# Performance work log

Hardware: AMD Instinct MI355X
Metric: run time of the kernel (lower is better)

## Reference

```python
import jax, jax.numpy as jnp
import numpy as np

B, S, I, H, O = 64, 2048, 128, 256, 128


def setup_inputs() -> dict:
    key = jax.random.key(0)
    ks = jax.random.split(key, 7)
    s = 1.0 / np.sqrt(H)
    return {
        "x": jax.random.normal(ks[0], (B, S, I), dtype=jnp.float32),
        "W_ih": jax.random.uniform(ks[1], (H, I), jnp.float32, -s, s),
        "W_hh": jax.random.uniform(ks[2], (H, H), jnp.float32, -s, s),
        "b_ih": jax.random.uniform(ks[3], (H,), jnp.float32, -s, s),
        "b_hh": jax.random.uniform(ks[4], (H,), jnp.float32, -s, s),
        "W_fc": jax.random.uniform(ks[5], (O, H), jnp.float32, -s, s),
        "b_fc": jax.random.uniform(ks[6], (O,), jnp.float32, -s, s),
    }


def reference(x, W_ih, W_hh, b_ih, b_hh, W_fc, b_fc):
    # h_t = tanh(x_t @ W_ih^T + h_{t-1} @ W_hh^T + b_ih + b_hh)
    b = b_ih + b_hh
    # Precompute input projection for all timesteps in one GEMM: [B,S,H]
    xproj = jnp.einsum('bsi,hi->bsh', x, W_ih) + b

    def step(h, xp_t):  # h: [B,H], xp_t: [B,H]
        h_next = jnp.tanh(xp_t + h @ W_hh.T)
        return h_next, h_next

    h0 = jnp.zeros((B, H), dtype=x.dtype)
    _, hs = jax.lax.scan(step, h0, jnp.swapaxes(xproj, 0, 1))  # hs: [S,B,H]
    hidden_states = jnp.swapaxes(hs, 0, 1)  # [B,S,H]
    outputs = jnp.einsum('bsh,oh->bso', hidden_states, W_fc) + b_fc  # [B,S,O]
    return outputs, hidden_states
```

## Files before the change

kernel.cpp:

```cpp
#include <hip/hip_runtime.h>

#define BB 64
#define SS 2048
#define II 128
#define HH 256
#define OO 128

typedef _Float16 h2_t __attribute__((ext_vector_type(2)));

__device__ __forceinline__ h2_t u2h(unsigned u) {
    union { unsigned u; h2_t h; } c; c.u = u; return c.h;
}

#if __has_builtin(__builtin_amdgcn_fdot2)
__device__ __forceinline__ float fdot2(unsigned h, unsigned w, float acc) {
    return __builtin_amdgcn_fdot2(u2h(h), u2h(w), acc, false);
}
#else
__device__ __forceinline__ float fdot2(unsigned h, unsigned w, float acc) {
    h2_t hh = u2h(h), ww = u2h(w);
    acc = fmaf((float)hh.x, (float)ww.x, acc);
    acc = fmaf((float)hh.y, (float)ww.y, acc);
    return acc;
}
#endif

__global__ void prep_kernel(const float* __restrict__ W_ih, const float* __restrict__ b_ih,
                            const float* __restrict__ b_hh, const float* __restrict__ W_fc,
                            float* __restrict__ wihT, float* __restrict__ wfcT,
                            float* __restrict__ biasc, unsigned* __restrict__ whh16,
                            const float* __restrict__ W_hh) {
    int idx = blockIdx.x * 256 + threadIdx.x;
    if (idx < HH * II) {
        int j = idx / II, k = idx % II;
        wihT[k * HH + j] = W_ih[idx];
    }
    if (idx < OO * HH) {
        int j = idx / HH, k = idx % HH;
        wfcT[k * OO + j] = W_fc[idx];
    }
    if (idx < HH * (HH / 2)) {
        int j = idx / (HH / 2), i = idx % (HH / 2);
        union { h2_t h; unsigned u; } pk;
        pk.h.x = (_Float16)W_hh[j * HH + 2 * i];
        pk.h.y = (_Float16)W_hh[j * HH + 2 * i + 1];
        whh16[idx] = pk.u;
    }
    if (idx < HH) biasc[idx] = b_ih[idx] + b_hh[idx];
}

template<int KD, int JD, int RT>
__global__ __launch_bounds__(256, 2)
void gemm_rk(const float* __restrict__ A, const float* __restrict__ Wt,
             const float* __restrict__ bias, float* __restrict__ C) {
    constexpr int KT = 64;
    constexpr int TJ = JD / 8;
    constexpr int TR = RT / 8;
    static_assert(TJ * TR == 256, "bad tiling");

    __shared__ __align__(16) float a_lds[RT][KT];
    __shared__ __align__(16) float w_lds[KT][JD];

    const int tid = threadIdx.x;
    const int tj = tid % TJ;
    const int tr = tid / TJ;
    const long r0 = (long)blockIdx.x * RT;

    float acc[8][8];
#pragma unroll
    for (int r = 0; r < 8; ++r)
#pragma unroll
        for (int j = 0; j < 8; ++j) acc[r][j] = 0.0f;

    for (int kt = 0; kt < KD; kt += KT) {
        {
            constexpr int NF4 = RT * KT / 4;
#pragma unroll
            for (int f = 0; f < NF4 / 256; ++f) {
                int fl = f * 256 + tid;
                int rr = fl / (KT / 4), kk4 = fl % (KT / 4);
                *(float4*)&a_lds[rr][kk4 * 4] =
                    *(const float4*)&A[(r0 + rr) * KD + kt + kk4 * 4];
            }
        }
        {
            constexpr int NF4 = KT * JD / 4;
#pragma unroll
            for (int f = 0; f < NF4 / 256; ++f) {
                int fl = f * 256 + tid;
                int kk = fl / (JD / 4), jj4 = fl % (JD / 4);
                *(float4*)&w_lds[kk][jj4 * 4] =
                    *(const float4*)&Wt[(long)(kt + kk) * JD + jj4 * 4];
            }
        }
        __syncthreads();

#pragma unroll 4
        for (int k4 = 0; k4 < KT; k4 += 4) {
            float4 xv[8];
#pragma unroll
            for (int r = 0; r < 8; ++r)
                xv[r] = *(const float4*)&a_lds[tr * 8 + r][k4];
#pragma unroll
            for (int i = 0; i < 4; ++i) {
                float4 wa = *(const float4*)&w_lds[k4 + i][tj * 8];
                float4 wb = *(const float4*)&w_lds[k4 + i][tj * 8 + 4];
#pragma unroll
                for (int r = 0; r < 8; ++r) {
                    float xs = (i == 0) ? xv[r].x : (i == 1) ? xv[r].y
                             : (i == 2) ? xv[r].z : xv[r].w;
                    acc[r][0] = fmaf(xs, wa.x, acc[r][0]);
                    acc[r][1] = fmaf(xs, wa.y, acc[r][1]);
                    acc[r][2] = fmaf(xs, wa.z, acc[r][2]);
                    acc[r][3] = fmaf(xs, wa.w, acc[r][3]);
                    acc[r][4] = fmaf(xs, wb.x, acc[r][4]);
                    acc[r][5] = fmaf(xs, wb.y, acc[r][5]);
                    acc[r][6] = fmaf(xs, wb.z, acc[r][6]);
                    acc[r][7] = fmaf(xs, wb.w, acc[r][7]);
                }
            }
        }
        __syncthreads();
    }

    float4 b0 = *(const float4*)&bias[tj * 8];
    float4 b1 = *(const float4*)&bias[tj * 8 + 4];
#pragma unroll
    for (int r = 0; r < 8; ++r) {
        long row = r0 + tr * 8 + r;
        float4 o0, o1;
        o0.x = acc[r][0] + b0.x; o0.y = acc[r][1] + b0.y;
        o0.z = acc[r][2] + b0.z; o0.w = acc[r][3] + b0.w;
        o1.x = acc[r][4] + b1.x; o1.y = acc[r][5] + b1.y;
        o1.z = acc[r][6] + b1.z; o1.w = acc[r][7] + b1.w;
        *(float4*)&C[row * JD + tj * 8]     = o0;
        *(float4*)&C[row * JD + tj * 8 + 4] = o1;
    }
}

__global__ __attribute__((amdgpu_waves_per_eu(2, 2))) __launch_bounds__(512)
void rnn_scan(const unsigned* __restrict__ whh16, float* __restrict__ hid) {
    const int b   = blockIdx.x;
    const int tid = threadIdx.x;
    const int w   = tid >> 6;
    const int l   = tid & 63;
    const int sl  = l & 15;
    const int q   = l >> 4;

    const int j0 = w * 32 + sl * 2;

    __shared__ __align__(16) unsigned h16[2][4 * 36];

    uint4 wA[8], wB[8];
#pragma unroll
    for (int i = 0; i < 8; ++i) {
        wA[i] = *(const uint4*)&whh16[(size_t)j0 * (HH / 2) + q * 32 + i * 4];
        wB[i] = *(const uint4*)&whh16[(size_t)(j0 + 1) * (HH / 2) + q * 32 + i * 4];
    }

    for (int i = tid; i < 2 * 4 * 36; i += 512) ((unsigned*)h16)[i] = 0u;

    float* __restrict__ base = hid + (size_t)b * SS * HH;
    float2 xp0 = *(const float2*)&base[j0];
    float2 xp1 = *(const float2*)&base[HH + j0];
    __syncthreads();

#pragma unroll 1
    for (int t = 0; t < SS; ++t) {
        float2 xp2 = make_float2(0.f, 0.f);
        if (t + 2 < SS) xp2 = *(const float2*)&base[(size_t)(t + 2) * HH + j0];

        const uint4* hb = (const uint4*)&h16[t & 1][q * 36];
        float aA0 = 0.f, aA1 = 0.f, aB0 = 0.f, aB1 = 0.f;
#pragma unroll
        for (int i = 0; i < 8; ++i) {
            uint4 hv = hb[i];
            aA0 = fdot2(hv.x, wA[i].x, aA0);
            aA1 = fdot2(hv.y, wA[i].y, aA1);
            aA0 = fdot2(hv.z, wA[i].z, aA0);
            aA1 = fdot2(hv.w, wA[i].w, aA1);
            aB0 = fdot2(hv.x, wB[i].x, aB0);
            aB1 = fdot2(hv.y, wB[i].y, aB1);
            aB0 = fdot2(hv.z, wB[i].z, aB0);
            aB1 = fdot2(hv.w, wB[i].w, aB1);
        }
        float sA = aA0 + aA1;
        float sB = aB0 + aB1;
        sA += __shfl_xor(sA, 16, 64);
        sA += __shfl_xor(sA, 32, 64);
        sB += __shfl_xor(sB, 16, 64);
        sB += __shfl_xor(sB, 32, 64);

        float s0 = xp0.x + sA;
        float s1 = xp0.y + sB;
        float e0  = __expf(2.0f * s0);
        float e1  = __expf(2.0f * s1);
        float hn0 = 1.0f - __fdividef(2.0f, e0 + 1.0f);
        float hn1 = 1.0f - __fdividef(2.0f, e1 + 1.0f);

        if (q == 0) {
            union { h2_t h; unsigned u; } pk;
            pk.h.x = (_Float16)hn0;
            pk.h.y = (_Float16)hn1;
            const int W = j0 >> 1;
            h16[(t & 1) ^ 1][(W >> 5) * 36 + (W & 31)] = pk.u;
            *(float2*)&base[(size_t)t * HH + j0] = make_float2(hn0, hn1);
        }
        __syncthreads();
        xp0 = xp1;
        xp1 = xp2;
    }
}

extern "C" void kernel_launch(void* const* d_in, const int* in_sizes, int n_in,
                              void* d_out, int out_size, void* d_ws, size_t ws_size,
                              hipStream_t stream) {
    const float* x    = (const float*)d_in[0];
    const float* W_ih = (const float*)d_in[1];
    const float* W_hh = (const float*)d_in[2];
    const float* b_ih = (const float*)d_in[3];
    const float* b_hh = (const float*)d_in[4];
    const float* W_fc = (const float*)d_in[5];
    const float* b_fc = (const float*)d_in[6];

    float* out_fc  = (float*)d_out;
    float* hidden  = (float*)d_out + (size_t)BB * SS * OO;

    float*    wihT  = (float*)d_ws;
    float*    wfcT  = wihT + II * HH;
    float*    biasc = wfcT + HH * OO;
    unsigned* whh16 = (unsigned*)(biasc + HH);

    const long NR = (long)BB * SS;

    prep_kernel<<<128, 256, 0, stream>>>(W_ih, b_ih, b_hh, W_fc,
                                         wihT, wfcT, biasc, whh16, W_hh);
    gemm_rk<II, HH, 64><<<NR / 64, 256, 0, stream>>>(x, wihT, biasc, hidden);
    rnn_scan<<<BB, 512, 0, stream>>>(whh16, hidden);
    gemm_rk<HH, OO, 128><<<NR / 128, 256, 0, stream>>>(hidden, wfcT, b_fc, out_fc);
}
```

Before: 1.582 ms.

## Batch 16 sequences per block and compute recurrence with MFMA

Rewrites the recurrent scan so each block processes 16 batch elements together, computing h@W_hh^T with 16x16x32 fp16 MFMA instructions instead of per-thread fdot2 plus cross-lane shuffle reductions. The grid shrinks from 64 to 4 blocks. The intent is to cut per-step latency by using matrix cores and removing shuffles, at the cost of more tanh work per thread, dependent MFMA chains, and far fewer active CUs.

```diff
diff --git a/kernel.cpp b/kernel.cpp
--- a/kernel.cpp
+++ b/kernel.cpp
@@ -5,25 +5,12 @@
 #define II 128
 #define HH 256
 #define OO 128
-
-typedef _Float16 h2_t __attribute__((ext_vector_type(2)));
-
-__device__ __forceinline__ h2_t u2h(unsigned u) {
-    union { unsigned u; h2_t h; } c; c.u = u; return c.h;
-}
-
-#if __has_builtin(__builtin_amdgcn_fdot2)
-__device__ __forceinline__ float fdot2(unsigned h, unsigned w, float acc) {
-    return __builtin_amdgcn_fdot2(u2h(h), u2h(w), acc, false);
-}
-#else
-__device__ __forceinline__ float fdot2(unsigned h, unsigned w, float acc) {
-    h2_t hh = u2h(h), ww = u2h(w);
-    acc = fmaf((float)hh.x, (float)ww.x, acc);
-    acc = fmaf((float)hh.y, (float)ww.y, acc);
-    return acc;
-}
-#endif
+#define GG 16
+#define RS 264
+
+typedef _Float16 half8 __attribute__((ext_vector_type(8)));
+typedef float    f32x4 __attribute__((ext_vector_type(4)));
+typedef _Float16 h2_t  __attribute__((ext_vector_type(2)));
 
 __global__ void prep_kernel(const float* __restrict__ W_ih, const float* __restrict__ b_ih,
                             const float* __restrict__ b_hh, const float* __restrict__ W_fc,
@@ -138,77 +125,83 @@
     }
 }
 
+__device__ __forceinline__ float tanh_fast(float s) {
+    float e = __expf(2.0f * s);
+    return 1.0f - __fdividef(2.0f, e + 1.0f);
+}
+
 __global__ __attribute__((amdgpu_waves_per_eu(2, 2))) __launch_bounds__(512)
 void rnn_scan(const unsigned* __restrict__ whh16, float* __restrict__ hid) {
-    const int b   = blockIdx.x;
+    const int bg  = blockIdx.x;
     const int tid = threadIdx.x;
     const int w   = tid >> 6;
     const int l   = tid & 63;
-    const int sl  = l & 15;
+    const int r16 = l & 15;
     const int q   = l >> 4;
 
-    const int j0 = w * 32 + sl * 2;
-
-    __shared__ __align__(16) unsigned h16[2][4 * 36];
-
-    uint4 wA[8], wB[8];
-#pragma unroll
-    for (int i = 0; i < 8; ++i) {
-        wA[i] = *(const uint4*)&whh16[(size_t)j0 * (HH / 2) + q * 32 + i * 4];
-        wB[i] = *(const uint4*)&whh16[(size_t)(j0 + 1) * (HH / 2) + q * 32 + i * 4];
-    }
-
-    for (int i = tid; i < 2 * 4 * 36; i += 512) ((unsigned*)h16)[i] = 0u;
-
-    float* __restrict__ base = hid + (size_t)b * SS * HH;
-    float2 xp0 = *(const float2*)&base[j0];
-    float2 xp1 = *(const float2*)&base[HH + j0];
+    __shared__ __align__(16) _Float16 h16[2][GG][RS];
+
+    half8 a_f[2][8];
+#pragma unroll
+    for (int rt = 0; rt < 2; ++rt) {
+        const unsigned* wp = &whh16[(w * 32 + rt * 16 + r16) * (HH / 2)];
+#pragma unroll
+        for (int kt = 0; kt < 8; ++kt)
+            a_f[rt][kt] = *(const half8*)&wp[kt * 16 + q * 4];
+    }
+
+    for (int i = tid; i < 2 * GG * RS / 2; i += 512) ((unsigned*)h16)[i] = 0u;
+
+    const int c = r16;
+    float* __restrict__ basec = hid + (size_t)(bg * GG + c) * SS * HH;
+    const int row0 = w * 32 + q * 4;
+
+    f32x4 xA0 = *(const f32x4*)(basec + row0);
+    f32x4 xB0 = *(const f32x4*)(basec + row0 + 16);
+    f32x4 xA1 = *(const f32x4*)(basec + HH + row0);
+    f32x4 xB1 = *(const f32x4*)(basec + HH + row0 + 16);
     __syncthreads();
 
+    int cur = 0;
 #pragma unroll 1
     for (int t = 0; t < SS; ++t) {
-        float2 xp2 = make_float2(0.f, 0.f);
-        if (t + 2 < SS) xp2 = *(const float2*)&base[(size_t)(t + 2) * HH + j0];
-
-        const uint4* hb = (const uint4*)&h16[t & 1][q * 36];
-        float aA0 = 0.f, aA1 = 0.f, aB0 = 0.f, aB1 = 0.f;
-#pragma unroll
-        for (int i = 0; i < 8; ++i) {
-            uint4 hv = hb[i];
-            aA0 = fdot2(hv.x, wA[i].x, aA0);
-            aA1 = fdot2(hv.y, wA[i].y, aA1);
-            aA0 = fdot2(hv.z, wA[i].z, aA0);
-            aA1 = fdot2(hv.w, wA[i].w, aA1);
-            aB0 = fdot2(hv.x, wB[i].x, aB0);
-            aB1 = fdot2(hv.y, wB[i].y, aB1);
-            aB0 = fdot2(hv.z, wB[i].z, aB0);
-            aB1 = fdot2(hv.w, wB[i].w, aB1);
-        }
-        float sA = aA0 + aA1;
-        float sB = aB0 + aB1;
-        sA += __shfl_xor(sA, 16, 64);
-        sA += __shfl_xor(sA, 32, 64);
-        sB += __shfl_xor(sB, 16, 64);
-        sB += __shfl_xor(sB, 32, 64);
-
-        float s0 = xp0.x + sA;
-        float s1 = xp0.y + sB;
-        float e0  = __expf(2.0f * s0);
-        float e1  = __expf(2.0f * s1);
-        float hn0 = 1.0f - __fdividef(2.0f, e0 + 1.0f);
-        float hn1 = 1.0f - __fdividef(2.0f, e1 + 1.0f);
-
-        if (q == 0) {
-            union { h2_t h; unsigned u; } pk;
-            pk.h.x = (_Float16)hn0;
-            pk.h.y = (_Float16)hn1;
-            const int W = j0 >> 1;
-            h16[(t & 1) ^ 1][(W >> 5) * 36 + (W & 31)] = pk.u;
-            *(float2*)&base[(size_t)t * HH + j0] = make_float2(hn0, hn1);
-        }
+        f32x4 xA2 = {0.f, 0.f, 0.f, 0.f}, xB2 = xA2;
+        if (t + 2 < SS) {
+            xA2 = *(const f32x4*)(basec + (size_t)(t + 2) * HH + row0);
+            xB2 = *(const f32x4*)(basec + (size_t)(t + 2) * HH + row0 + 16);
+        }
+
+        f32x4 acc0 = {0.f, 0.f, 0.f, 0.f}, acc1 = acc0;
+#pragma unroll
+        for (int kt = 0; kt < 8; ++kt) {
+            half8 bf = *(const half8*)&h16[cur][c][kt * 32 + q * 8];
+            acc0 = __builtin_amdgcn_mfma_f32_16x16x32_f16(a_f[0][kt], bf, acc0, 0, 0, 0);
+            acc1 = __builtin_amdgcn_mfma_f32_16x16x32_f16(a_f[1][kt], bf, acc1, 0, 0, 0);
+        }
+        acc0 += xA0;
+        acc1 += xB0;
+
+        f32x4 h0, h1;
+        h0.x = tanh_fast(acc0.x); h0.y = tanh_fast(acc0.y);
+        h0.z = tanh_fast(acc0.z); h0.w = tanh_fast(acc0.w);
+        h1.x = tanh_fast(acc1.x); h1.y = tanh_fast(acc1.y);
+        h1.z = tanh_fast(acc1.z); h1.w = tanh_fast(acc1.w);
+
+        *(f32x4*)(basec + (size_t)t * HH + row0)      = h0;
+        *(f32x4*)(basec + (size_t)t * HH + row0 + 16) = h1;
+
+        union { _Float16 h[4]; uint2 v; } p0, p1;
+        p0.h[0] = (_Float16)h0.x; p0.h[1] = (_Float16)h0.y;
+        p0.h[2] = (_Float16)h0.z; p0.h[3] = (_Float16)h0.w;
+        p1.h[0] = (_Float16)h1.x; p1.h[1] = (_Float16)h1.y;
+        p1.h[2] = (_Float16)h1.z; p1.h[3] = (_Float16)h1.w;
+        *(uint2*)&h16[cur ^ 1][c][row0]      = p0.v;
+        *(uint2*)&h16[cur ^ 1][c][row0 + 16] = p1.v;
+
         __syncthreads();
-        xp0 = xp1;
-        xp1 = xp2;
+        cur ^= 1;
+        xA0 = xA1; xA1 = xA2;
+        xB0 = xB1; xB1 = xB2;
     }
 }
 
@@ -236,6 +229,6 @@
     prep_kernel<<<128, 256, 0, stream>>>(W_ih, b_ih, b_hh, W_fc,
                                          wihT, wfcT, biasc, whh16, W_hh);
     gemm_rk<II, HH, 64><<<NR / 64, 256, 0, stream>>>(x, wihT, biasc, hidden);
-    rnn_scan<<<BB, 512, 0, stream>>>(whh16, hidden);
+    rnn_scan<<<BB / GG, 512, 0, stream>>>(whh16, hidden);
     gemm_rk<HH, OO, 128><<<NR / 128, 256, 0, stream>>>(hidden, wfcT, b_fc, out_fc);
 }
```

Result: slower. 2.208 ms (+39.6%).

## Stream swizzled fp16 W_hh from cache every step instead of holding in registers

Applied to the files above, without the earlier changes.

The recurrent weight matrix is repacked in the prep kernel into a lane-coalesced swizzled layout, and the scan kernel reloads each thread's 16 uint4 weight slices from global memory (L1/L2) on every timestep instead of keeping them resident in registers. This cuts register pressure, which may improve scheduling or avoid spills, but adds 256 bytes of loads per thread on the serial critical path of every step.

```diff
diff --git a/kernel.cpp b/kernel.cpp
--- a/kernel.cpp
+++ b/kernel.cpp
@@ -28,7 +28,7 @@
 __global__ void prep_kernel(const float* __restrict__ W_ih, const float* __restrict__ b_ih,
                             const float* __restrict__ b_hh, const float* __restrict__ W_fc,
                             float* __restrict__ wihT, float* __restrict__ wfcT,
-                            float* __restrict__ biasc, unsigned* __restrict__ whh16,
+                            float* __restrict__ biasc, unsigned* __restrict__ wsw,
                             const float* __restrict__ W_hh) {
     int idx = blockIdx.x * 256 + threadIdx.x;
     if (idx < HH * II) {
@@ -40,11 +40,19 @@
         wfcT[k * OO + j] = W_fc[idx];
     }
     if (idx < HH * (HH / 2)) {
-        int j = idx / (HH / 2), i = idx % (HH / 2);
+        int d   = idx & 3;
+        int s   = idx >> 2;
+        int l   = s & 63;
+        int rem = s >> 6;
+        int i    = rem & 7;
+        int pair = (rem >> 3) & 1;
+        int w    = rem >> 4;
+        int j    = w * 32 + (l & 15) * 2 + pair;
+        int word = (l >> 4) * 32 + i * 4 + d;
         union { h2_t h; unsigned u; } pk;
-        pk.h.x = (_Float16)W_hh[j * HH + 2 * i];
-        pk.h.y = (_Float16)W_hh[j * HH + 2 * i + 1];
-        whh16[idx] = pk.u;
+        pk.h.x = (_Float16)W_hh[j * HH + 2 * word];
+        pk.h.y = (_Float16)W_hh[j * HH + 2 * word + 1];
+        wsw[idx] = pk.u;
     }
     if (idx < HH) biasc[idx] = b_ih[idx] + b_hh[idx];
 }
@@ -139,7 +147,7 @@
 }
 
 __global__ __attribute__((amdgpu_waves_per_eu(2, 2))) __launch_bounds__(512)
-void rnn_scan(const unsigned* __restrict__ whh16, float* __restrict__ hid) {
+void rnn_scan(const unsigned* __restrict__ wsw, float* __restrict__ hid) {
     const int b   = blockIdx.x;
     const int tid = threadIdx.x;
     const int w   = tid >> 6;
@@ -151,12 +159,7 @@
 
     __shared__ __align__(16) unsigned h16[2][4 * 36];
 
-    uint4 wA[8], wB[8];
-#pragma unroll
-    for (int i = 0; i < 8; ++i) {
-        wA[i] = *(const uint4*)&whh16[(size_t)j0 * (HH / 2) + q * 32 + i * 4];
-        wB[i] = *(const uint4*)&whh16[(size_t)(j0 + 1) * (HH / 2) + q * 32 + i * 4];
-    }
+    const uint4* __restrict__ wp = (const uint4*)wsw + ((size_t)w << 10) + l;
 
     for (int i = tid; i < 2 * 4 * 36; i += 512) ((unsigned*)h16)[i] = 0u;
 
@@ -167,6 +170,13 @@
 
 #pragma unroll 1
     for (int t = 0; t < SS; ++t) {
+        uint4 wA[8], wB[8];
+#pragma unroll
+        for (int i = 0; i < 8; ++i) {
+            wA[i] = wp[i * 64];
+            wB[i] = wp[(8 + i) * 64];
+        }
+
         float2 xp2 = make_float2(0.f, 0.f);
         if (t + 2 < SS) xp2 = *(const float2*)&base[(size_t)(t + 2) * HH + j0];
 
@@ -229,13 +239,13 @@
     float*    wihT  = (float*)d_ws;
     float*    wfcT  = wihT + II * HH;
     float*    biasc = wfcT + HH * OO;
-    unsigned* whh16 = (unsigned*)(biasc + HH);
+    unsigned* wsw   = (unsigned*)(biasc + HH);
 
     const long NR = (long)BB * SS;
 
     prep_kernel<<<128, 256, 0, stream>>>(W_ih, b_ih, b_hh, W_fc,
-                                         wihT, wfcT, biasc, whh16, W_hh);
+                                         wihT, wfcT, biasc, wsw, W_hh);
     gemm_rk<II, HH, 64><<<NR / 64, 256, 0, stream>>>(x, wihT, biasc, hidden);
-    rnn_scan<<<BB, 512, 0, stream>>>(whh16, hidden);
+    rnn_scan<<<BB, 512, 0, stream>>>(wsw, hidden);
     gemm_rk<HH, OO, 128><<<NR / 128, 256, 0, stream>>>(hidden, wfcT, b_fc, out_fc);
 }
```

After: 1.456 ms. -8.0%, faster.
